# Performance work log

Hardware: AMD Instinct MI355X
Metric: run time of the kernel (lower is better)

## Reference

```python
import jax, jax.numpy as jnp
import numpy as np

NEG_SLOPE = 0.2  # PyG GATConv default


def gat_layer(x, src, dst, W, a_src, a_dst, bias, n_nodes, heads, out_c, concat):
    # x: [N, F_in]; W: [F_in, heads*out_c]; a_src/a_dst: [heads, out_c]
    h = (x @ W).reshape(n_nodes, heads, out_c)            # [N,H,C]
    alpha_src = jnp.einsum('nhc,hc->nh', h, a_src)         # [N,H]
    alpha_dst = jnp.einsum('nhc,hc->nh', h, a_dst)         # [N,H]
    logits = jax.nn.leaky_relu(alpha_src[src] + alpha_dst[dst], NEG_SLOPE)  # [E,H]
    # segment softmax over incoming edges of each dst node
    m = jax.ops.segment_max(logits, dst, num_segments=n_nodes)
    ex = jnp.exp(logits - m[dst])
    denom = jax.ops.segment_sum(ex, dst, num_segments=n_nodes)
    alpha = ex / denom[dst]                                # [E,H]
    msg = h[src] * alpha[:, :, None]                       # [E,H,C]
    out = jax.ops.segment_sum(msg, dst, num_segments=n_nodes)  # [N,H,C]
    if concat:
        out = out.reshape(n_nodes, heads * out_c)
    else:
        out = out.mean(axis=1)
    return out + bias


def setup_inputs() -> dict:
    key = jax.random.key(0)
    ks = jax.random.split(key, 12)
    N, E, F_IN, OUT_C, NG = 50000, 1600000, 64, 32, 512
    H1, C1 = 4, 32
    x = jax.random.normal(ks[0], (N, F_IN), dtype=jnp.float32)
    edge_index = jax.random.randint(ks[1], (2, E), 0, N, dtype=jnp.int64)
    batch = jnp.sort(jax.random.randint(ks[2], (N,), 0, NG, dtype=jnp.int64))
    s1 = 1.0 / np.sqrt(F_IN)
    W1 = jax.random.uniform(ks[3], (F_IN, H1 * C1), jnp.float32, -s1, s1)
    a_src1 = jax.random.uniform(ks[4], (H1, C1), jnp.float32, -s1, s1)
    a_dst1 = jax.random.uniform(ks[5], (H1, C1), jnp.float32, -s1, s1)
    b1 = jnp.zeros((H1 * C1,), jnp.float32)
    s2 = 1.0 / np.sqrt(H1 * C1)
    W2 = jax.random.uniform(ks[6], (H1 * C1, OUT_C), jnp.float32, -s2, s2)
    a_src2 = jax.random.uniform(ks[7], (1, OUT_C), jnp.float32, -s2, s2)
    a_dst2 = jax.random.uniform(ks[8], (1, OUT_C), jnp.float32, -s2, s2)
    b2 = jnp.zeros((OUT_C,), jnp.float32)
    return {"x": x, "edge_index": edge_index, "batch": batch, "num_graphs": NG,
            "W1": W1, "a_src1": a_src1, "a_dst1": a_dst1, "b1": b1,
            "W2": W2, "a_src2": a_src2, "a_dst2": a_dst2, "b2": b2}


def reference(x, edge_index, batch, num_graphs, W1, a_src1, a_dst1, b1, W2, a_src2, a_dst2, b2):
    N = x.shape[0]
    loops = jnp.arange(N, dtype=edge_index.dtype)
    src = jnp.concatenate([edge_index[0], loops])  # add_self_loops=True (PyG default)
    dst = jnp.concatenate([edge_index[1], loops])
    h = gat_layer(x, src, dst, W1, a_src1, a_dst1, b1, N, 4, 32, True)
    h = jax.nn.elu(h)
    h = gat_layer(h, src, dst, W2, a_src2, a_dst2, b2, N, 1, 32, False)
    # global_mean_pool over graph ids
    sums = jax.ops.segment_sum(h, batch, num_segments=num_graphs)
    counts = jax.ops.segment_sum(jnp.ones((N,), h.dtype), batch, num_segments=num_graphs)
    return sums / jnp.maximum(counts, 1.0)[:, None]
```

## Files before the change

kernel.cpp:

```cpp
#include <hip/hip_runtime.h>
#include <hip/hip_bf16.h>

#define N_NODES     50000
#define N_EDGES     1600000
#define N_TOT_EDGES (N_EDGES + N_NODES)
#define NUM_GRAPHS  512
#define F_IN        64
#define F1          128
#define C2          32
#define NEG_SLOPE   0.2f

#define BSH         6
#define NB          ((N_NODES + 63) >> 6)
#define BIN_T       256
#define EPB         8192
#define NBLK        ((N_TOT_EDGES + EPB - 1) / EPB)
#define EPT         (EPB / BIN_T)
#define CAPB        2560
#define CAP         6144
#define G1B         (N_NODES / 8)

typedef __hip_bfloat16 bf16;
typedef unsigned int uint32;
typedef unsigned short ushort;

static __device__ __forceinline__ float bf2f(bf16 v) { return __bfloat162float(v); }
static __device__ __forceinline__ ushort f2bf_bits(float f) {
    __hip_bfloat16 h = __float2bfloat16(f);
    union { __hip_bfloat16 h; ushort u; } c; c.h = h; return c.u;
}
static __device__ __forceinline__ float bflo(uint32 u) { return __uint_as_float(u << 16); }
static __device__ __forceinline__ float bfhi(uint32 u) { return __uint_as_float(u & 0xFFFF0000u); }

static __device__ __forceinline__ float fload(const void* p, int i, bool f32) {
    return f32 ? ((const float*)p)[i] : bf2f(((const bf16*)p)[i]);
}
static __device__ __forceinline__ int iload(const void* p, int i, bool i64) {
    return i64 ? (int)((const long long*)p)[i] : ((const int*)p)[i];
}
static __device__ __forceinline__ float lrelu(float l) { return l > 0.f ? l : NEG_SLOPE * l; }
static __device__ __forceinline__ int clampn(int s) {
    return s < 0 ? 0 : (s >= N_NODES ? N_NODES - 1 : s);
}

__global__ void sniff_kernel(const ushort* __restrict__ xb, const int* __restrict__ ei,
                             int* __restrict__ flags, int* __restrict__ cursor) {
    int t = threadIdx.x;
    if (t < 16) flags[t] = 0;
    for (int b = t; b < NB; b += 256) cursor[b] = 0;
    __syncthreads();
    int badf = 0;
    for (int i = t; i < 8192; i += 256) {
        int e = (xb[i] >> 7) & 0xFF;
        if (e >= 0xC0) badf = 1;
    }
    if (badf) atomicOr(&flags[0], 1);
    if (ei[2 * t + 1] != 0) atomicOr(&flags[1], 1);
}

__global__ __launch_bounds__(256) void prep_kernel(
    const void* __restrict__ ei, const void* __restrict__ x, const void* __restrict__ W1,
    const void* __restrict__ awS, const void* __restrict__ awD,
    const int* __restrict__ flags,
    int* __restrict__ cursor, uint32* __restrict__ packed,
    bf16* __restrict__ h1, float* __restrict__ as1, float* __restrict__ ad1) {
    __shared__ int lcnt[NB];
    __shared__ int loff[NB];
    __shared__ int runB[NB];
    __shared__ float xs[8][F_IN];
    bool f32 = (flags[0] != 0);
    bool i64 = (flags[1] == 0);
    int tid = threadIdx.x;

    if (blockIdx.x < (unsigned)NBLK) {
        for (int b = tid; b < NB; b += BIN_T) { lcnt[b] = 0; loff[b] = 0; }
        __syncthreads();
        int e0 = blockIdx.x * EPB;
        uint32 pkreg[EPT];
#pragma unroll
        for (int it = 0; it < EPT; ++it) {
            int e = e0 + it * BIN_T + tid;
            if (e < N_TOT_EDGES) {
                int s, d;
                if (e < N_EDGES) { s = clampn(iload(ei, e, i64)); d = clampn(iload(ei, N_EDGES + e, i64)); }
                else             { s = d = e - N_EDGES; }
                pkreg[it] = ((uint32)d << 16) | (uint32)s;
                atomicAdd(&lcnt[d >> BSH], 1);
            } else {
                pkreg[it] = 0xFFFFFFFFu;
            }
        }
        __syncthreads();
        for (int b = tid; b < NB; b += BIN_T)
            runB[b] = lcnt[b] ? atomicAdd(&cursor[b], lcnt[b]) : 0;
        __syncthreads();
#pragma unroll
        for (int it = 0; it < EPT; ++it) {
            uint32 pk = pkreg[it];
            if (pk != 0xFFFFFFFFu) {
                int b = pk >> 22;
                int r = runB[b] + atomicAdd(&loff[b], 1);
                if (r >= CAPB) r = CAPB - 1;
                packed[(size_t)b * CAPB + r] = pk;
            }
        }
    } else {
        int n0 = (blockIdx.x - NBLK) * 8;
        int hi = tid >> 7, f = tid & 127;
        if (f32) {
            for (int i = tid; i < 8 * F_IN; i += 256)
                xs[i >> 6][i & 63] = ((const float*)x)[(size_t)n0 * F_IN + i];
        } else {
            const uint32* xu = (const uint32*)x + (size_t)n0 * 32;
            uint32 u = xu[tid];
            int row = tid >> 5, c2 = (tid & 31) * 2;
            xs[row][c2]     = bflo(u);
            xs[row][c2 + 1] = bfhi(u);
        }
        __syncthreads();
        float acc0 = 0.f, acc1 = 0.f, acc2 = 0.f, acc3 = 0.f;
        const float* xr0 = xs[hi * 4 + 0];
        const float* xr1 = xs[hi * 4 + 1];
        const float* xr2 = xs[hi * 4 + 2];
        const float* xr3 = xs[hi * 4 + 3];
        if (f32) {
            const float* w = (const float*)W1;
#pragma unroll
            for (int k = 0; k < F_IN; ++k) {
                float wv = w[k * F1 + f];
                acc0 += xr0[k] * wv; acc1 += xr1[k] * wv;
                acc2 += xr2[k] * wv; acc3 += xr3[k] * wv;
            }
        } else {
            const bf16* w = (const bf16*)W1;
#pragma unroll
            for (int k = 0; k < F_IN; ++k) {
                float wv = bf2f(w[k * F1 + f]);
                acc0 += xr0[k] * wv; acc1 += xr1[k] * wv;
                acc2 += xr2[k] * wv; acc3 += xr3[k] * wv;
            }
        }
        float aws = fload(awS, f, f32), awd = fload(awD, f, f32);
        float accs[4] = {acc0, acc1, acc2, acc3};
        int h = (f >> 5), c = f & 31;
#pragma unroll
        for (int j = 0; j < 4; ++j) {
            int n = n0 + hi * 4 + j;
            h1[(size_t)n * F1 + f] = __float2bfloat16(accs[j]);
            float ps = accs[j] * aws, pd = accs[j] * awd;
#pragma unroll
            for (int off = 16; off > 0; off >>= 1) {
                ps += __shfl_down(ps, off, 32);
                pd += __shfl_down(pd, off, 32);
            }
            if (c == 0) {
                as1[n * 4 + h] = ps;
                ad1[n * 4 + h] = pd;
            }
        }
    }
}

__global__ __launch_bounds__(1024) void bucket_scan_kernel(
    const int* __restrict__ counts, int* __restrict__ bucketBase) {
    __shared__ int lds[1024];
    int t = threadIdx.x;
    int v = (t < NB) ? counts[t] : 0;
    lds[t] = v;
    __syncthreads();
    for (int off = 1; off < 1024; off <<= 1) {
        int u = (t >= off) ? lds[t - off] : 0;
        __syncthreads();
        lds[t] += u;
        __syncthreads();
    }
    if (t < NB) bucketBase[t] = lds[t] - v;
    if (t == NB - 1) bucketBase[NB] = lds[t];
}

__global__ __launch_bounds__(256) void build_kernel(
    const uint32* __restrict__ packed, const int* __restrict__ bucketBase,
    int* __restrict__ rowptr, int* __restrict__ col) {
    __shared__ int ncnt[64];
    __shared__ int nbase[64];
    __shared__ int ncur[64];
    __shared__ int colL[CAP];
    int b = blockIdx.x, tid = threadIdx.x;
    int base = bucketBase[b];
    int cnt = bucketBase[b + 1] - base;
    if (cnt < 0) cnt = 0;
    if (cnt > CAPB) cnt = CAPB;
    int n0 = b << BSH;
    const uint32* pk = packed + (size_t)b * CAPB;
    if (tid < 64) ncnt[tid] = 0;
    __syncthreads();
    uint32 pkr[(CAPB + 255) / 256];
    int m = 0;
    for (int i = tid; i < cnt; i += 256) {
        pkr[m] = pk[i];
        atomicAdd(&ncnt[(pkr[m] >> 16) & 63], 1);
        ++m;
    }
    __syncthreads();
    if (tid == 0) {
        int run = 0;
        for (int j = 0; j < 64; ++j) { nbase[j] = run; ncur[j] = run; run += ncnt[j]; }
    }
    __syncthreads();
    if (tid < 64 && n0 + tid < N_NODES) rowptr[n0 + tid] = base + nbase[tid];
    if (b == 0 && tid == 96) rowptr[N_NODES] = N_TOT_EDGES;
    bool staged = (cnt <= CAP);
    m = 0;
    for (int i = tid; i < cnt; i += 256) {
        uint32 u = pkr[m++];
        int r = atomicAdd(&ncur[(u >> 16) & 63], 1);
        if (staged) colL[r] = (int)(u & 0xFFFFu);
        else        col[base + r] = (int)(u & 0xFFFFu);
    }
    __syncthreads();
    if (staged)
        for (int i = tid; i < cnt; i += 256) col[base + i] = colL[i];
}

__global__ __launch_bounds__(256) void agg1_kernel(
    const bf16* __restrict__ h1, const float* __restrict__ as1, const float* __restrict__ ad1,
    const int* __restrict__ rowptr, const int* __restrict__ col,
    const void* __restrict__ b1, const int* __restrict__ flags, bf16* __restrict__ y1) {
    __shared__ float4 wbuf[4][64];
    __shared__ int    scol[4][64];
    bool f32 = (flags[0] != 0);
    int tid = threadIdx.x, lane = tid & 63, wv = tid >> 6;
    int n = blockIdx.x * 4 + wv;
    int r0 = rowptr[n], r1 = rowptr[n + 1];
    float4 ad = ((const float4*)ad1)[n];
    const uint4* h1q = (const uint4*)h1;
    int slot = lane >> 4, cl = lane & 15;
    int hsel = cl >> 2;
    const float* wfb = (const float*)&wbuf[wv][0];
    float acc[8] = {0.f,0.f,0.f,0.f,0.f,0.f,0.f,0.f};
    float den = 0.f;

    for (int base = r0; base < r1; base += 64) {
        int cnt = r1 - base; if (cnt > 64) cnt = 64;
        int idx = lane < cnt ? lane : cnt - 1;
        int s = clampn(col[base + idx]);
        float4 a = ((const float4*)as1)[s];
        float4 w;
        w.x = __expf(lrelu(a.x + ad.x));
        w.y = __expf(lrelu(a.y + ad.y));
        w.z = __expf(lrelu(a.z + ad.z));
        w.w = __expf(lrelu(a.w + ad.w));
        wbuf[wv][lane] = w;
        scol[wv][lane] = s;
        __builtin_amdgcn_wave_barrier();
        int i = slot;
        for (; i + 4 < cnt; i += 8) {
            float we0 = wfb[i * 4 + hsel];
            int   s0  = scol[wv][i];
            float we1 = wfb[(i + 4) * 4 + hsel];
            int   s1  = scol[wv][i + 4];
            uint4 u0 = h1q[(size_t)s0 * 16 + cl];
            uint4 u1 = h1q[(size_t)s1 * 16 + cl];
            acc[0] += we0 * bflo(u0.x); acc[1] += we0 * bfhi(u0.x);
            acc[2] += we0 * bflo(u0.y); acc[3] += we0 * bfhi(u0.y);
            acc[4] += we0 * bflo(u0.z); acc[5] += we0 * bfhi(u0.z);
            acc[6] += we0 * bflo(u0.w); acc[7] += we0 * bfhi(u0.w);
            den += we0;
            acc[0] += we1 * bflo(u1.x); acc[1] += we1 * bfhi(u1.x);
            acc[2] += we1 * bflo(u1.y); acc[3] += we1 * bfhi(u1.y);
            acc[4] += we1 * bflo(u1.z); acc[5] += we1 * bfhi(u1.z);
            acc[6] += we1 * bflo(u1.w); acc[7] += we1 * bfhi(u1.w);
            den += we1;
        }
        for (; i < cnt; i += 4) {
            float we = wfb[i * 4 + hsel];
            int si = scol[wv][i];
            uint4 u = h1q[(size_t)si * 16 + cl];
            acc[0] += we * bflo(u.x); acc[1] += we * bfhi(u.x);
            acc[2] += we * bflo(u.y); acc[3] += we * bfhi(u.y);
            acc[4] += we * bflo(u.z); acc[5] += we * bfhi(u.z);
            acc[6] += we * bflo(u.w); acc[7] += we * bfhi(u.w);
            den += we;
        }
        __builtin_amdgcn_wave_barrier();
    }
#pragma unroll
    for (int off = 16; off <= 32; off <<= 1) {
#pragma unroll
        for (int j = 0; j < 8; ++j) acc[j] += __shfl_xor(acc[j], off, 64);
        den += __shfl_xor(den, off, 64);
    }
    if (lane < 16) {
        float rd = 1.f / den;
        int c0 = lane * 8;
        uint4 st;
        uint32 pk[4];
#pragma unroll
        for (int j = 0; j < 4; ++j) {
            float oa = acc[2 * j]     * rd + fload(b1, c0 + 2 * j, f32);
            float ob = acc[2 * j + 1] * rd + fload(b1, c0 + 2 * j + 1, f32);
            oa = oa > 0.f ? oa : (__expf(oa) - 1.f);
            ob = ob > 0.f ? ob : (__expf(ob) - 1.f);
            pk[j] = (uint32)f2bf_bits(oa) | ((uint32)f2bf_bits(ob) << 16);
        }
        st.x = pk[0]; st.y = pk[1]; st.z = pk[2]; st.w = pk[3];
        ((uint4*)y1)[(size_t)n * 16 + lane] = st;
    }
}

__global__ __launch_bounds__(128) void gemm2_kernel(
    const bf16* __restrict__ y1, const void* __restrict__ W2,
    const void* __restrict__ aS, const void* __restrict__ aD,
    const int* __restrict__ flags,
    bf16* __restrict__ h2, float* __restrict__ as2, float* __restrict__ ad2) {
    bool f32 = (flags[0] != 0);
    __shared__ float ys[4][F1];
    __shared__ float part[4][F1];
    int n0 = blockIdx.x * 4, tid = threadIdx.x, c = tid & 31, q = tid >> 5;
    const uint32* yu = (const uint32*)y1 + (size_t)n0 * 64;
#pragma unroll
    for (int i = tid; i < 256; i += 128) {
        uint32 u = yu[i];
        int row = i >> 6, pos = (i & 63) * 2;
        ys[row][pos]     = bflo(u);
        ys[row][pos + 1] = bfhi(u);
    }
    __syncthreads();
    float wr[32];
    if (f32) {
        const float* w = (const float*)W2;
#pragma unroll
        for (int k = 0; k < 32; ++k) wr[k] = w[(q * 32 + k) * C2 + c];
    } else {
        const bf16* w = (const bf16*)W2;
#pragma unroll
        for (int k = 0; k < 32; ++k) wr[k] = bf2f(w[(q * 32 + k) * C2 + c]);
    }
    float a0 = 0.f, a1 = 0.f, a2 = 0.f, a3 = 0.f;
#pragma unroll
    for (int k = 0; k < 32; ++k) {
        int f = q * 32 + k;
        float wv = wr[k];
        a0 += ys[0][f] * wv; a1 += ys[1][f] * wv;
        a2 += ys[2][f] * wv; a3 += ys[3][f] * wv;
    }
    part[0][tid] = a0; part[1][tid] = a1; part[2][tid] = a2; part[3][tid] = a3;
    __syncthreads();
    if (q == 0) {
        float vs = fload(aS, c, f32), vd = fload(aD, c, f32);
#pragma unroll
        for (int j = 0; j < 4; ++j) {
            float s = part[j][c] + part[j][32 + c] + part[j][64 + c] + part[j][96 + c];
            h2[(size_t)(n0 + j) * C2 + c] = __float2bfloat16(s);
            float ps = s * vs, pd = s * vd;
#pragma unroll
            for (int off = 16; off > 0; off >>= 1) {
                ps += __shfl_down(ps, off, 32);
                pd += __shfl_down(pd, off, 32);
            }
            if (c == 0) { as2[n0 + j] = ps; ad2[n0 + j] = pd; }
        }
    }
}

__global__ __launch_bounds__(256) void agg2_kernel(
    const bf16* __restrict__ h2, const float* __restrict__ as2, const float* __restrict__ ad2,
    const int* __restrict__ rowptr, const int* __restrict__ col,
    const void* __restrict__ b2, const int* __restrict__ flags, float* __restrict__ v2) {
    __shared__ float wl[4][64];
    __shared__ int   sc[4][64];
    bool f32 = (flags[0] != 0);
    int tid = threadIdx.x, lane = tid & 63, wv = tid >> 6;
    int n = blockIdx.x * 4 + wv;
    int r0 = rowptr[n], r1 = rowptr[n + 1];
    float adn = ad2[n];
    const uint4* h2q = (const uint4*)h2;
    int slot = lane >> 2, cl = lane & 3;
    float acc[8] = {0.f,0.f,0.f,0.f,0.f,0.f,0.f,0.f};
    float den = 0.f;

    for (int base = r0; base < r1; base += 64) {
        int cnt = r1 - base; if (cnt > 64) cnt = 64;
        int idx = lane < cnt ? lane : cnt - 1;
        int s = clampn(col[base + idx]);
        wl[wv][lane] = __expf(lrelu(as2[s] + adn));
        sc[wv][lane] = s;
        __builtin_amdgcn_wave_barrier();
        int i = slot;
        for (; i + 16 < cnt; i += 32) {
            float w0 = wl[wv][i];        int s0 = sc[wv][i];
            float w1 = wl[wv][i + 16];   int s1 = sc[wv][i + 16];
            uint4 u0 = h2q[(size_t)s0 * 4 + cl];
            uint4 u1 = h2q[(size_t)s1 * 4 + cl];
            acc[0] += w0 * bflo(u0.x); acc[1] += w0 * bfhi(u0.x);
            acc[2] += w0 * bflo(u0.y); acc[3] += w0 * bfhi(u0.y);
            acc[4] += w0 * bflo(u0.z); acc[5] += w0 * bfhi(u0.z);
            acc[6] += w0 * bflo(u0.w); acc[7] += w0 * bfhi(u0.w);
            den += w0;
            acc[0] += w1 * bflo(u1.x); acc[1] += w1 * bfhi(u1.x);
            acc[2] += w1 * bflo(u1.y); acc[3] += w1 * bfhi(u1.y);
            acc[4] += w1 * bflo(u1.z); acc[5] += w1 * bfhi(u1.z);
            acc[6] += w1 * bflo(u1.w); acc[7] += w1 * bfhi(u1.w);
            den += w1;
        }
        for (; i < cnt; i += 16) {
            float w = wl[wv][i];
            int si = sc[wv][i];
            uint4 u = h2q[(size_t)si * 4 + cl];
            acc[0] += w * bflo(u.x); acc[1] += w * bfhi(u.x);
            acc[2] += w * bflo(u.y); acc[3] += w * bfhi(u.y);
            acc[4] += w * bflo(u.z); acc[5] += w * bfhi(u.z);
            acc[6] += w * bflo(u.w); acc[7] += w * bfhi(u.w);
            den += w;
        }
        __builtin_amdgcn_wave_barrier();
    }
#pragma unroll
    for (int off = 4; off <= 32; off <<= 1) {
#pragma unroll
        for (int j = 0; j < 8; ++j) acc[j] += __shfl_xor(acc[j], off, 64);
        den += __shfl_xor(den, off, 64);
    }
    if (lane < 4) {
        float rd = 1.f / den;
        int c0 = lane * 8;
        float4 o0, o1;
        o0.x = acc[0] * rd + fload(b2, c0 + 0, f32);
        o0.y = acc[1] * rd + fload(b2, c0 + 1, f32);
        o0.z = acc[2] * rd + fload(b2, c0 + 2, f32);
        o0.w = acc[3] * rd + fload(b2, c0 + 3, f32);
        o1.x = acc[4] * rd + fload(b2, c0 + 4, f32);
        o1.y = acc[5] * rd + fload(b2, c0 + 5, f32);
        o1.z = acc[6] * rd + fload(b2, c0 + 6, f32);
        o1.w = acc[7] * rd + fload(b2, c0 + 7, f32);
        ((float4*)v2)[(size_t)n * 8 + lane * 2]     = o0;
        ((float4*)v2)[(size_t)n * 8 + lane * 2 + 1] = o1;
    }
}

__global__ __launch_bounds__(64) void pool_kernel(
    const float* __restrict__ v2, const void* __restrict__ batch,
    const int* __restrict__ flags, void* __restrict__ out) {
    bool f32 = (flags[0] != 0);
    bool i64 = (flags[1] == 0);
    int g = blockIdx.x, lane = threadIdx.x;
    int lo = 0, hi = N_NODES;
    while (lo < hi) { int mid = (lo + hi) >> 1; if (iload(batch, mid, i64) < g) lo = mid + 1; else hi = mid; }
    int lo2 = lo, hi2 = N_NODES;
    while (lo2 < hi2) { int mid = (lo2 + hi2) >> 1; if (iload(batch, mid, i64) < g + 1) lo2 = mid + 1; else hi2 = mid; }
    int c = lane & 31, slot = lane >> 5;
    float sum = 0.f;
    for (int nn = lo + slot; nn < lo2; nn += 2) sum += v2[nn * C2 + c];
    sum += __shfl_down(sum, 32, 64);
    if (lane < 32) {
        int cntn = lo2 - lo; if (cntn < 1) cntn = 1;
        float v = sum / (float)cntn;
        if (f32) ((float*)out)[g * C2 + c] = v;
        else     ((bf16*)out)[g * C2 + c] = __float2bfloat16(v);
    }
}

extern "C" void kernel_launch(void* const* d_in, const int* in_sizes, int n_in,
                              void* d_out, int out_size, void* d_ws, size_t ws_size,
                              hipStream_t stream) {
    const void* x   = d_in[0];
    const void* ei  = d_in[1];
    const void* bat = d_in[2];
    const void* W1  = d_in[4];
    const void* aS1 = d_in[5];
    const void* aD1 = d_in[6];
    const void* b1  = d_in[7];
    const void* W2  = d_in[8];
    const void* aS2 = d_in[9];
    const void* aD2 = d_in[10];
    const void* b2  = d_in[11];

    char* p = (char*)d_ws;
    auto alloc = [&](size_t bytes) -> char* {
        char* r = p;
        p += (bytes + 255) & ~size_t(255);
        return r;
    };
    char* regionA = alloc((size_t)N_NODES * F1 * 2);
    char* regionB = alloc((size_t)N_NODES * F1 * 2);
    uint32* packed = (uint32*)alloc((size_t)NB * CAPB * 4);
    bf16*  h1   = (bf16*)regionA;
    bf16*  h2   = (bf16*)regionA;
    bf16*  y1   = (bf16*)regionB;
    float* v2   = (float*)regionB;
    float* as1    = (float*)alloc((size_t)N_NODES * 4 * 4);
    float* ad1    = (float*)alloc((size_t)N_NODES * 4 * 4);
    float* as2    = (float*)alloc((size_t)N_NODES * 4);
    float* ad2    = (float*)alloc((size_t)N_NODES * 4);
    int*   rowptr = (int*)alloc((size_t)(N_NODES + 1) * 4);
    int*   col    = (int*)alloc((size_t)N_TOT_EDGES * 4);
    int*   bucketBase = (int*)alloc((size_t)(NB + 1) * 4);
    int*   cursor = (int*)alloc((size_t)NB * 4);
    int*   flags  = (int*)alloc(64);

    sniff_kernel<<<1, 256, 0, stream>>>((const ushort*)x, (const int*)ei, flags, cursor);

    prep_kernel<<<NBLK + G1B, 256, 0, stream>>>(ei, x, W1, aS1, aD1, flags,
                                                cursor, packed, h1, as1, ad1);
    bucket_scan_kernel<<<1, 1024, 0, stream>>>(cursor, bucketBase);
    build_kernel<<<NB, 256, 0, stream>>>(packed, bucketBase, rowptr, col);

    agg1_kernel<<<N_NODES / 4, 256, 0, stream>>>(h1, as1, ad1, rowptr, col, b1, flags, y1);
    gemm2_kernel<<<N_NODES / 4, 128, 0, stream>>>(y1, W2, aS2, aD2, flags, h2, as2, ad2);
    agg2_kernel<<<N_NODES / 4, 256, 0, stream>>>(h2, as2, ad2, rowptr, col, b2, flags, v2);
    pool_kernel<<<NUM_GRAPHS, 64, 0, stream>>>(v2, bat, flags, d_out);
}
```

Measured before the change: 273.7 us.

## Fuse layer-2 GEMM into agg1 and fold bucket scan into build kernel

Removes the separate bucket_scan kernel by having each build block compute its own prefix sum over bucket counts with a block reduction. Fuses the second-layer linear transform and attention projections into agg1's epilogue, keeping the ELU output in shared memory instead of writing and rereading y1 as bf16. This drops two kernel launches and one round trip through global memory for the intermediate activations. In exchange, every build block redundantly reads the counts, agg1 uses more shared memory and adds block-wide barriers that may lower occupancy, and y1 is no longer rounded to bf16 before the GEMM.

Result: no change. 268.7 us (-1.8%).

```diff
diff --git a/kernel.cpp b/kernel.cpp
--- a/kernel.cpp
+++ b/kernel.cpp
@@ -25,10 +25,6 @@
 typedef unsigned short ushort;
 
 static __device__ __forceinline__ float bf2f(bf16 v) { return __bfloat162float(v); }
-static __device__ __forceinline__ ushort f2bf_bits(float f) {
-    __hip_bfloat16 h = __float2bfloat16(f);
-    union { __hip_bfloat16 h; ushort u; } c; c.h = h; return c.u;
-}
 static __device__ __forceinline__ float bflo(uint32 u) { return __uint_as_float(u << 16); }
 static __device__ __forceinline__ float bfhi(uint32 u) { return __uint_as_float(u & 0xFFFF0000u); }
 
@@ -161,34 +157,25 @@
     }
 }
 
-__global__ __launch_bounds__(1024) void bucket_scan_kernel(
-    const int* __restrict__ counts, int* __restrict__ bucketBase) {
-    __shared__ int lds[1024];
-    int t = threadIdx.x;
-    int v = (t < NB) ? counts[t] : 0;
-    lds[t] = v;
-    __syncthreads();
-    for (int off = 1; off < 1024; off <<= 1) {
-        int u = (t >= off) ? lds[t - off] : 0;
-        __syncthreads();
-        lds[t] += u;
-        __syncthreads();
-    }
-    if (t < NB) bucketBase[t] = lds[t] - v;
-    if (t == NB - 1) bucketBase[NB] = lds[t];
-}
-
 __global__ __launch_bounds__(256) void build_kernel(
-    const uint32* __restrict__ packed, const int* __restrict__ bucketBase,
+    const uint32* __restrict__ packed, const int* __restrict__ counts,
     int* __restrict__ rowptr, int* __restrict__ col) {
+    __shared__ int red[256];
     __shared__ int ncnt[64];
     __shared__ int nbase[64];
     __shared__ int ncur[64];
     __shared__ int colL[CAP];
     int b = blockIdx.x, tid = threadIdx.x;
-    int base = bucketBase[b];
-    int cnt = bucketBase[b + 1] - base;
-    if (cnt < 0) cnt = 0;
+    int prt = 0;
+    for (int i = tid; i < b; i += 256) prt += counts[i];
+    red[tid] = prt;
+    __syncthreads();
+    for (int off = 128; off > 0; off >>= 1) {
+        if (tid < off) red[tid] += red[tid + off];
+        __syncthreads();
+    }
+    int base = red[0];
+    int cnt = counts[b];
     if (cnt > CAPB) cnt = CAPB;
     int n0 = b << BSH;
     const uint32* pk = packed + (size_t)b * CAPB;
@@ -225,12 +212,18 @@
 __global__ __launch_bounds__(256) void agg1_kernel(
     const bf16* __restrict__ h1, const float* __restrict__ as1, const float* __restrict__ ad1,
     const int* __restrict__ rowptr, const int* __restrict__ col,
-    const void* __restrict__ b1, const int* __restrict__ flags, bf16* __restrict__ y1) {
+    const void* __restrict__ b1, const void* __restrict__ W2,
+    const void* __restrict__ aS2w, const void* __restrict__ aD2w,
+    const int* __restrict__ flags,
+    bf16* __restrict__ h2, float* __restrict__ as2, float* __restrict__ ad2) {
     __shared__ float4 wbuf[4][64];
     __shared__ int    scol[4][64];
+    __shared__ float  yL[4][F1];
+    __shared__ float  part[4][256];
     bool f32 = (flags[0] != 0);
     int tid = threadIdx.x, lane = tid & 63, wv = tid >> 6;
-    int n = blockIdx.x * 4 + wv;
+    int n0 = blockIdx.x * 4;
+    int n = n0 + wv;
     int r0 = rowptr[n], r1 = rowptr[n + 1];
     float4 ad = ((const float4*)ad1)[n];
     const uint4* h1q = (const uint4*)h1;
@@ -293,73 +286,52 @@
     if (lane < 16) {
         float rd = 1.f / den;
         int c0 = lane * 8;
-        uint4 st;
-        uint32 pk[4];
-#pragma unroll
-        for (int j = 0; j < 4; ++j) {
-            float oa = acc[2 * j]     * rd + fload(b1, c0 + 2 * j, f32);
-            float ob = acc[2 * j + 1] * rd + fload(b1, c0 + 2 * j + 1, f32);
-            oa = oa > 0.f ? oa : (__expf(oa) - 1.f);
-            ob = ob > 0.f ? ob : (__expf(ob) - 1.f);
-            pk[j] = (uint32)f2bf_bits(oa) | ((uint32)f2bf_bits(ob) << 16);
-        }
-        st.x = pk[0]; st.y = pk[1]; st.z = pk[2]; st.w = pk[3];
-        ((uint4*)y1)[(size_t)n * 16 + lane] = st;
-    }
-}
-
-__global__ __launch_bounds__(128) void gemm2_kernel(
-    const bf16* __restrict__ y1, const void* __restrict__ W2,
-    const void* __restrict__ aS, const void* __restrict__ aD,
-    const int* __restrict__ flags,
-    bf16* __restrict__ h2, float* __restrict__ as2, float* __restrict__ ad2) {
-    bool f32 = (flags[0] != 0);
-    __shared__ float ys[4][F1];
-    __shared__ float part[4][F1];
-    int n0 = blockIdx.x * 4, tid = threadIdx.x, c = tid & 31, q = tid >> 5;
-    const uint32* yu = (const uint32*)y1 + (size_t)n0 * 64;
-#pragma unroll
-    for (int i = tid; i < 256; i += 128) {
-        uint32 u = yu[i];
-        int row = i >> 6, pos = (i & 63) * 2;
-        ys[row][pos]     = bflo(u);
-        ys[row][pos + 1] = bfhi(u);
-    }
-    __syncthreads();
-    float wr[32];
-    if (f32) {
-        const float* w = (const float*)W2;
-#pragma unroll
-        for (int k = 0; k < 32; ++k) wr[k] = w[(q * 32 + k) * C2 + c];
-    } else {
-        const bf16* w = (const bf16*)W2;
-#pragma unroll
-        for (int k = 0; k < 32; ++k) wr[k] = bf2f(w[(q * 32 + k) * C2 + c]);
-    }
-    float a0 = 0.f, a1 = 0.f, a2 = 0.f, a3 = 0.f;
-#pragma unroll
-    for (int k = 0; k < 32; ++k) {
-        int f = q * 32 + k;
-        float wv = wr[k];
-        a0 += ys[0][f] * wv; a1 += ys[1][f] * wv;
-        a2 += ys[2][f] * wv; a3 += ys[3][f] * wv;
-    }
-    part[0][tid] = a0; part[1][tid] = a1; part[2][tid] = a2; part[3][tid] = a3;
-    __syncthreads();
-    if (q == 0) {
-        float vs = fload(aS, c, f32), vd = fload(aD, c, f32);
-#pragma unroll
-        for (int j = 0; j < 4; ++j) {
-            float s = part[j][c] + part[j][32 + c] + part[j][64 + c] + part[j][96 + c];
-            h2[(size_t)(n0 + j) * C2 + c] = __float2bfloat16(s);
-            float ps = s * vs, pd = s * vd;
-#pragma unroll
-            for (int off = 16; off > 0; off >>= 1) {
-                ps += __shfl_down(ps, off, 32);
-                pd += __shfl_down(pd, off, 32);
-            }
-            if (c == 0) { as2[n0 + j] = ps; ad2[n0 + j] = pd; }
-        }
+#pragma unroll
+        for (int j = 0; j < 8; ++j) {
+            float o = acc[j] * rd + fload(b1, c0 + j, f32);
+            yL[wv][c0 + j] = o > 0.f ? o : (__expf(o) - 1.f);
+        }
+    }
+    __syncthreads();
+    {
+        int c = tid & 31, q = tid >> 5;
+        float wr[16];
+        if (f32) {
+            const float* w = (const float*)W2;
+#pragma unroll
+            for (int k = 0; k < 16; ++k) wr[k] = w[(q * 16 + k) * C2 + c];
+        } else {
+            const bf16* w = (const bf16*)W2;
+#pragma unroll
+            for (int k = 0; k < 16; ++k) wr[k] = bf2f(w[(q * 16 + k) * C2 + c]);
+        }
+        float p0 = 0.f, p1 = 0.f, p2 = 0.f, p3 = 0.f;
+#pragma unroll
+        for (int k = 0; k < 16; ++k) {
+            int f = q * 16 + k;
+            float wvv = wr[k];
+            p0 += yL[0][f] * wvv;
+            p1 += yL[1][f] * wvv;
+            p2 += yL[2][f] * wvv;
+            p3 += yL[3][f] * wvv;
+        }
+        part[0][tid] = p0; part[1][tid] = p1; part[2][tid] = p2; part[3][tid] = p3;
+    }
+    __syncthreads();
+    if (tid < 128) {
+        int j = tid >> 5, cc = tid & 31;
+        float s = 0.f;
+#pragma unroll
+        for (int qq = 0; qq < 8; ++qq) s += part[j][qq * 32 + cc];
+        h2[(size_t)(n0 + j) * C2 + cc] = __float2bfloat16(s);
+        float ps = s * fload(aS2w, cc, f32);
+        float pd = s * fload(aD2w, cc, f32);
+#pragma unroll
+        for (int off = 16; off > 0; off >>= 1) {
+            ps += __shfl_down(ps, off, 32);
+            pd += __shfl_down(pd, off, 32);
+        }
+        if (cc == 0) { as2[n0 + j] = ps; ad2[n0 + j] = pd; }
     }
 }
 
@@ -485,16 +457,14 @@
     char* regionB = alloc((size_t)N_NODES * F1 * 2);
     uint32* packed = (uint32*)alloc((size_t)NB * CAPB * 4);
     bf16*  h1   = (bf16*)regionA;
-    bf16*  h2   = (bf16*)regionA;
-    bf16*  y1   = (bf16*)regionB;
-    float* v2   = (float*)regionB;
+    bf16*  h2   = (bf16*)regionB;
+    float* v2   = (float*)(regionB + (size_t)N_NODES * C2 * 2);
     float* as1    = (float*)alloc((size_t)N_NODES * 4 * 4);
     float* ad1    = (float*)alloc((size_t)N_NODES * 4 * 4);
     float* as2    = (float*)alloc((size_t)N_NODES * 4);
     float* ad2    = (float*)alloc((size_t)N_NODES * 4);
     int*   rowptr = (int*)alloc((size_t)(N_NODES + 1) * 4);
     int*   col    = (int*)alloc((size_t)N_TOT_EDGES * 4);
-    int*   bucketBase = (int*)alloc((size_t)(NB + 1) * 4);
     int*   cursor = (int*)alloc((size_t)NB * 4);
     int*   flags  = (int*)alloc(64);
 
@@ -502,11 +472,10 @@
 
     prep_kernel<<<NBLK + G1B, 256, 0, stream>>>(ei, x, W1, aS1, aD1, flags,
                                                 cursor, packed, h1, as1, ad1);
-    bucket_scan_kernel<<<1, 1024, 0, stream>>>(cursor, bucketBase);
-    build_kernel<<<NB, 256, 0, stream>>>(packed, bucketBase, rowptr, col);
-
-    agg1_kernel<<<N_NODES / 4, 256, 0, stream>>>(h1, as1, ad1, rowptr, col, b1, flags, y1);
-    gemm2_kernel<<<N_NODES / 4, 128, 0, stream>>>(y1, W2, aS2, aD2, flags, h2, as2, ad2);
+    build_kernel<<<NB, 256, 0, stream>>>(packed, cursor, rowptr, col);
+
+    agg1_kernel<<<N_NODES / 4, 256, 0, stream>>>(h1, as1, ad1, rowptr, col, b1, W2, aS2, aD2,
+                                                 flags, h2, as2, ad2);
     agg2_kernel<<<N_NODES / 4, 256, 0, stream>>>(h2, as2, ad2, rowptr, col, b2, flags, v2);
     pool_kernel<<<NUM_GRAPHS, 64, 0, stream>>>(v2, bat, flags, d_out);
 }
```
